# Optimization experiments

Measured on AMD Instinct MI355X. Metric: run time of the kernel, lower is better.

## Reference

```python
import jax, jax.numpy as jnp
import numpy as np

N = 100000   # nodes
E = 3200000  # edges
F = 128      # in = hidden = out channels
V = 8        # virtual nodes
L = 3        # conv layers
EPS = 1e-5


def setup_inputs() -> dict:
    key = jax.random.key(0)
    ks = jax.random.split(key, 16)
    rn = lambda k, s, sc=0.05: jax.random.normal(k, s, jnp.float32) * sc
    return {
        "x": rn(ks[0], (N, F), 1.0),
        "edge_index": jax.random.randint(ks[1], (2, E), 0, N, jnp.int32),
        "vn_mask": jax.random.randint(ks[2], (V, N), 0, 2, jnp.int32).astype(bool),
        "Wc": rn(ks[3], (L, F, F)),
        "bc": rn(ks[4], (L, F)),
        "bn_g": jnp.ones((L, F), jnp.float32),
        "bn_b": jnp.zeros((L, F), jnp.float32),
        "vn_embed": rn(ks[5], (V, F)),
        "mlp_W1": rn(ks[6], (L - 1, V, F, 2 * F)),
        "mlp_b1": rn(ks[7], (L - 1, V, 2 * F)),
        "ln1_g": jnp.ones((L - 1, V, 2 * F), jnp.float32),
        "ln1_b": jnp.zeros((L - 1, V, 2 * F), jnp.float32),
        "mlp_W2": rn(ks[8], (L - 1, V, 2 * F, F)),
        "mlp_b2": rn(ks[9], (L - 1, V, F)),
        "ln2_g": jnp.ones((L - 1, V, F), jnp.float32),
        "ln2_b": jnp.zeros((L - 1, V, F), jnp.float32),
    }


def _ln(h, g, b):
    m = h.mean(-1, keepdims=True)
    v = ((h - m) ** 2).mean(-1, keepdims=True)
    return (h - m) * jax.lax.rsqrt(v + EPS) * g + b


def _bn(h, g, b):  # training-mode batch stats over nodes (dropout p=0)
    m = h.mean(0)
    v = ((h - m) ** 2).mean(0)
    return (h - m) * jax.lax.rsqrt(v + EPS) * g + b


def reference(x, edge_index, vn_mask, Wc, bc, bn_g, bn_b, vn_embed,
              mlp_W1, mlp_b1, ln1_g, ln1_b, mlp_W2, mlp_b2, ln2_g, ln2_b):
    src, dst = edge_index[0], edge_index[1]
    loops = jnp.arange(N, dtype=src.dtype)
    src_f = jnp.concatenate([src, loops])   # GCN adds self-loops
    dst_f = jnp.concatenate([dst, loops])
    deg = jax.ops.segment_sum(jnp.ones(src_f.shape[0], x.dtype), dst_f, num_segments=N)
    dinv = jnp.where(deg > 0, jax.lax.rsqrt(deg), 0.0)
    norm = dinv[src_f] * dinv[dst_f]        # sym-normalized edge weights

    def gcn(h, W, b):  # PyG GCNConv: linear -> normalized scatter-sum -> bias
        hl = h @ W
        out = jax.ops.segment_sum(hl[src_f] * norm[:, None], dst_f, num_segments=N)
        return out + b

    maskf = vn_mask.astype(x.dtype)  # [V, N]
    vn = vn_embed                    # [V, F]
    embs = [x]
    for layer in range(L):
        h = embs[layer] + vn.sum(0, keepdims=True)       # aggregation='sum'
        h = gcn(h, Wc[layer], bc[layer])
        h = _bn(h, bn_g[layer], bn_b[layer])
        if layer != L - 1:
            h = jax.nn.relu(h)
        embs.append(h)
        if layer < L - 1:
            pooled = maskf @ embs[layer]                 # per-VN global_add_pool
            tmp = pooled + vn
            h1 = jax.nn.relu(jnp.einsum('vf,vfh->vh', tmp, mlp_W1[layer]) + mlp_b1[layer])
            h1 = _ln(h1, ln1_g[layer], ln1_b[layer])
            h2 = jax.nn.relu(jnp.einsum('vh,vhf->vf', h1, mlp_W2[layer]) + mlp_b2[layer])
            vn = _ln(h2, ln2_g[layer], ln2_b[layer])
    return embs[-1]  # JK='last'
```

## Files before the change

### kernel.cpp

```cpp
#include <hip/hip_runtime.h>
#include <hip/hip_bf16.h>
#include <hip/hip_fp16.h>

#define NN 100000
#define EE 3200000
#define FF 128
#define F2 256
#define VV 8
#define LL 3
#define EPSV 1e-5f
#define NB 98
#define NTILES 3125

typedef _Float16 f16x8 __attribute__((ext_vector_type(8)));
typedef float f32x4 __attribute__((ext_vector_type(4)));

static inline int idiv(int a, int b){ return (a + b - 1) / b; }

__global__ void k_deg(const int* __restrict__ dst, int* __restrict__ edeg){
  int stride = gridDim.x * 256;
  for (int e = blockIdx.x * 256 + threadIdx.x; e < EE; e += stride)
    atomicAdd(&edeg[dst[e]], 1);
}

__global__ void k_scanA(const int* __restrict__ edeg, int* __restrict__ offs,
                        int* __restrict__ bsum, float* __restrict__ dinv){
  __shared__ int s[1024];
  int t = threadIdx.x;
  int i = blockIdx.x * 1024 + t;
  int v = (i < NN) ? edeg[i] : 0;
  if (i < NN) dinv[i] = rsqrtf((float)(v + 1));
  int x = v;
  s[t] = x; __syncthreads();
  for (int d = 1; d < 1024; d <<= 1){
    int y = (t >= d) ? s[t - d] : 0;
    __syncthreads();
    x += y; s[t] = x;
    __syncthreads();
  }
  if (i < NN) offs[i] = x - v;
  if (t == 1023) bsum[blockIdx.x] = x;
}

__global__ void k_scanB(int* __restrict__ bsum){
  __shared__ int s[128];
  int t = threadIdx.x;
  s[t] = (t < NB) ? bsum[t] : 0;
  __syncthreads();
  if (t == 0){
    int run = 0;
    for (int k = 0; k < NB; ++k){ int tmp = s[k]; s[k] = run; run += tmp; }
  }
  __syncthreads();
  if (t < NB) bsum[t] = s[t];
}

__global__ void k_scanC(int* __restrict__ offs, const int* __restrict__ bsum,
                        int* __restrict__ cursor){
  int i = blockIdx.x * 256 + threadIdx.x;
  if (i < NN){
    int o = offs[i] + bsum[i >> 10];
    offs[i] = o;
    cursor[i] = o;
  }
  if (i == 0) offs[NN] = EE;
}

__global__ void k_scatter(const int* __restrict__ src, const int* __restrict__ dst,
                          int* __restrict__ cursor, int* __restrict__ ssorted){
  int stride = gridDim.x * 256;
  for (int e = blockIdx.x * 256 + threadIdx.x; e < EE; e += stride){
    int d = dst[e];
    int pos = atomicAdd(&cursor[d], 1);
    ssorted[pos] = src[e];
  }
}

__global__ void k_maskdetect(const unsigned char* __restrict__ m, int* __restrict__ flag){
  int any = 0;
  for (int t = threadIdx.x; t < 4096; t += 256)
    if ((t & 3) && m[t]) any = 1;
  if (any) atomicOr(flag, 1);
}

__launch_bounds__(256)
__global__ void k_matmul(const float* __restrict__ in, const float* __restrict__ W,
                         const float* __restrict__ vn, const float* __restrict__ dinv,
                         const float* __restrict__ ss, int hasbn,
                         uint2* __restrict__ hlb){
  __shared__ _Float16 As[32 * 136];
  __shared__ float   Cs[32 * 132];
  __shared__ float vs[FF], rv[FF], scs[FF], shs[FF];
  int tid = threadIdx.x, lane = tid & 63, w = tid >> 6;
  if (tid < FF){
    float s = 0.f;
    for (int v = 0; v < VV; ++v) s += vn[v * FF + tid];
    vs[tid] = s;
    scs[tid] = hasbn ? ss[tid] : 1.0f;
    shs[tid] = hasbn ? ss[FF + tid] : 0.0f;
  }
  __syncthreads();
  if (tid < FF){
    float a = 0.f;
    for (int k = 0; k < FF; ++k) a += vs[k] * W[k * FF + tid];
    rv[tid] = a;
  }
  f16x8 Bf[4][2];
  int kg = (lane >> 4) * 8;
  int cl = lane & 15;
  #pragma unroll
  for (int q = 0; q < 4; ++q)
    #pragma unroll
    for (int ct = 0; ct < 2; ++ct){
      int col = (w * 2 + ct) * 16 + cl;
      #pragma unroll
      for (int j = 0; j < 8; ++j)
        Bf[q][ct][j] = (_Float16)W[(q * 32 + kg + j) * FF + col];
    }
  __syncthreads();

  for (int t = blockIdx.x; t < NTILES; t += gridDim.x){
    int base = t * 32;
    for (int i = tid; i < 32 * 32; i += 256){
      int r = i >> 5, cq = i & 31;
      float4 v = ((const float4*)(in + (size_t)(base + r) * FF))[cq];
      if (hasbn){
        int c0 = cq * 4;
        v.x = fmaxf(fmaf(v.x, scs[c0 + 0], shs[c0 + 0]), 0.f);
        v.y = fmaxf(fmaf(v.y, scs[c0 + 1], shs[c0 + 1]), 0.f);
        v.z = fmaxf(fmaf(v.z, scs[c0 + 2], shs[c0 + 2]), 0.f);
        v.w = fmaxf(fmaf(v.w, scs[c0 + 3], shs[c0 + 3]), 0.f);
      }
      _Float16* ap = &As[r * 136 + cq * 4];
      ap[0] = (_Float16)v.x; ap[1] = (_Float16)v.y;
      ap[2] = (_Float16)v.z; ap[3] = (_Float16)v.w;
    }
    __syncthreads();
    f32x4 acc[2][2] = {{{0,0,0,0},{0,0,0,0}},{{0,0,0,0},{0,0,0,0}}};
    #pragma unroll
    for (int q = 0; q < 4; ++q){
      f16x8 Af[2];
      #pragma unroll
      for (int rt = 0; rt < 2; ++rt)
        Af[rt] = *(const f16x8*)&As[(rt * 16 + cl) * 136 + q * 32 + kg];
      #pragma unroll
      for (int rt = 0; rt < 2; ++rt)
        #pragma unroll
        for (int ct = 0; ct < 2; ++ct)
          acc[rt][ct] = __builtin_amdgcn_mfma_f32_16x16x32_f16(Af[rt], Bf[q][ct], acc[rt][ct], 0, 0, 0);
    }
    #pragma unroll
    for (int rt = 0; rt < 2; ++rt)
      #pragma unroll
      for (int ct = 0; ct < 2; ++ct){
        int col = (w * 2 + ct) * 16 + cl;
        int r0 = rt * 16 + (lane >> 4) * 4;
        #pragma unroll
        for (int reg = 0; reg < 4; ++reg)
          Cs[(r0 + reg) * 132 + col] = acc[rt][ct][reg];
      }
    __syncthreads();
    for (int i = tid; i < 32 * 32; i += 256){
      int r = i >> 5, cq = i & 31;
      float d = dinv[base + r];
      float4 c = *(const float4*)&Cs[r * 132 + cq * 4];
      int c0 = cq * 4;
      float a0 = (c.x + rv[c0 + 0]) * d;
      float a1 = (c.y + rv[c0 + 1]) * d;
      float a2 = (c.z + rv[c0 + 2]) * d;
      float a3 = (c.w + rv[c0 + 3]) * d;
      __half2 h01 = __floats2half2_rn(a0, a1);
      __half2 h23 = __floats2half2_rn(a2, a3);
      uint2 pk;
      pk.x = *reinterpret_cast<unsigned int*>(&h01);
      pk.y = *reinterpret_cast<unsigned int*>(&h23);
      hlb[(size_t)(base + r) * 32 + cq] = pk;
    }
    __syncthreads();
  }
}

__launch_bounds__(256)
__global__ void k_gather(const unsigned int* __restrict__ hlb, const float* __restrict__ dinv,
                         const int* __restrict__ offs, const int* __restrict__ ssorted,
                         float2* __restrict__ agg2, float* __restrict__ stats){
  int tid = threadIdx.x;
  int lane = tid & 63;
  int wid = (blockIdx.x * 256 + tid) >> 6;
  int nw = (gridDim.x * 256) >> 6;
  float s0 = 0.f, s1 = 0.f, q0 = 0.f, q1 = 0.f;
  for (int n = wid; n < NN; n += nw){
    int off0 = offs[n], off1 = offs[n + 1];
    unsigned int ps = hlb[(size_t)n * 64 + lane];
    float2 acc = __half22float2(*reinterpret_cast<__half2*>(&ps));
    #pragma unroll 8
    for (int e = off0; e < off1; ++e){
      unsigned int p = hlb[(size_t)ssorted[e] * 64 + lane];
      float2 f = __half22float2(*reinterpret_cast<__half2*>(&p));
      acc.x += f.x; acc.y += f.y;
    }
    float dv = dinv[n];
    float v0 = acc.x * dv, v1 = acc.y * dv;
    agg2[(size_t)n * 64 + lane] = make_float2(v0, v1);
    s0 += v0; s1 += v1; q0 += v0 * v0; q1 += v1 * v1;
  }
  __shared__ float4 red[256];
  red[tid] = make_float4(s0, s1, q0, q1);
  __syncthreads();
  if (tid < 64){
    float4 a = red[tid], b = red[tid + 64], c = red[tid + 128], d = red[tid + 192];
    a.x += b.x + c.x + d.x; a.y += b.y + c.y + d.y;
    a.z += b.z + c.z + d.z; a.w += b.w + c.w + d.w;
    atomicAdd(&stats[2 * tid], a.x);
    atomicAdd(&stats[2 * tid + 1], a.y);
    atomicAdd(&stats[FF + 2 * tid], a.z);
    atomicAdd(&stats[FF + 2 * tid + 1], a.w);
  }
}

__global__ void k_bnfin(const float* __restrict__ stats, const float* __restrict__ g,
                        const float* __restrict__ b, float* __restrict__ ss){
  int j = threadIdx.x;
  float mean = stats[j] * (1.0f / NN);
  float var  = stats[FF + j] * (1.0f / NN) - mean * mean;
  float sc = rsqrtf(var + EPSV) * g[j];
  ss[j] = sc;
  ss[FF + j] = b[j] - mean * sc;
}

__launch_bounds__(256)
__global__ void k_bnapply(float4* __restrict__ h, const float* __restrict__ stats,
                          const float* __restrict__ g, const float* __restrict__ b){
  __shared__ float ss[2 * FF];
  int tid = threadIdx.x;
  if (tid < FF){
    float mean = stats[tid] * (1.0f / NN);
    float var  = stats[FF + tid] * (1.0f / NN) - mean * mean;
    float sc = rsqrtf(var + EPSV) * g[tid];
    ss[tid] = sc;
    ss[FF + tid] = b[tid] - mean * sc;
  }
  __syncthreads();
  int n4 = NN * FF / 4;
  int stride = gridDim.x * 256;
  for (int i = blockIdx.x * 256 + tid; i < n4; i += stride){
    int c = (i & 31) * 4;
    float4 v = h[i];
    float4 sc = *(const float4*)&ss[c];
    float4 sh = *(const float4*)&ss[FF + c];
    v.x = v.x * sc.x + sh.x;
    v.y = v.y * sc.y + sh.y;
    v.z = v.z * sc.z + sh.z;
    v.w = v.w * sc.w + sh.w;
    h[i] = v;
  }
}

__global__ void k_pool(const float* __restrict__ emb, const unsigned char* __restrict__ m8,
                       const int* __restrict__ m32, const int* __restrict__ flag,
                       const float* __restrict__ ss, int hasbn,
                       float* __restrict__ pooled){
  int isb = *flag;
  int tid = blockIdx.x * 256 + threadIdx.x;
  int j = tid & 127;
  int r = tid >> 7;
  int rs = (gridDim.x * 256) >> 7;
  float sc = hasbn ? ss[j] : 1.0f;
  float sh = hasbn ? ss[FF + j] : 0.0f;
  float acc[VV];
  #pragma unroll
  for (int v = 0; v < VV; ++v) acc[v] = 0.f;
  for (; r < NN; r += rs){
    float xv = emb[r * FF + j];
    xv = fmaf(xv, sc, sh);
    if (hasbn) xv = fmaxf(xv, 0.f);
    #pragma unroll
    for (int v = 0; v < VV; ++v){
      int mv = isb ? (int)m8[v * NN + r] : m32[v * NN + r];
      if (mv) acc[v] += xv;
    }
  }
  #pragma unroll
  for (int v = 0; v < VV; ++v) atomicAdd(&pooled[v * FF + j], acc[v]);
}

__device__ __forceinline__ float blockSum(float x, float* red, int tid){
  red[tid] = x; __syncthreads();
  #pragma unroll
  for (int s = 128; s >= 1; s >>= 1){
    if (tid < s) red[tid] += red[tid + s];
    __syncthreads();
  }
  float r = red[0];
  __syncthreads();
  return r;
}

__launch_bounds__(256)
__global__ void k_vnmlp(const float* __restrict__ pooled, const float* __restrict__ vnin,
                        const float* __restrict__ W1, const float* __restrict__ b1,
                        const float* __restrict__ g1, const float* __restrict__ bb1,
                        const float* __restrict__ W2, const float* __restrict__ b2,
                        const float* __restrict__ g2, const float* __restrict__ bb2,
                        float* __restrict__ vnout){
  int v = blockIdx.x;
  int tid = threadIdx.x;
  __shared__ float tmp_s[FF];
  __shared__ float h1_s[F2];
  __shared__ float red[256];
  if (tid < FF) tmp_s[tid] = pooled[v * FF + tid] + vnin[v * FF + tid];
  __syncthreads();
  const float* W1v = W1 + (size_t)v * FF * F2;
  float acc = b1[v * F2 + tid];
  for (int k = 0; k < FF; ++k) acc += tmp_s[k] * W1v[k * F2 + tid];
  acc = fmaxf(acc, 0.f);
  float sum = blockSum(acc, red, tid);
  float sq  = blockSum(acc * acc, red, tid);
  float mean = sum * (1.f / F2);
  float var  = sq * (1.f / F2) - mean * mean;
  float y = (acc - mean) * rsqrtf(var + EPSV) * g1[v * F2 + tid] + bb1[v * F2 + tid];
  h1_s[tid] = y;
  __syncthreads();
  const float* W2v = W2 + (size_t)v * F2 * FF;
  float h2 = 0.f;
  if (tid < FF){
    float a2 = b2[v * FF + tid];
    for (int k = 0; k < F2; ++k) a2 += h1_s[k] * W2v[k * FF + tid];
    h2 = fmaxf(a2, 0.f);
  }
  float sum2 = blockSum((tid < FF) ? h2 : 0.f, red, tid);
  float sq2  = blockSum((tid < FF) ? h2 * h2 : 0.f, red, tid);
  float mean2 = sum2 * (1.f / FF);
  float var2  = sq2 * (1.f / FF) - mean2 * mean2;
  if (tid < FF)
    vnout[v * FF + tid] = (h2 - mean2) * rsqrtf(var2 + EPSV) * g2[v * FF + tid]
                          + bb2[v * FF + tid];
}

extern "C" void kernel_launch(void* const* d_in, const int* in_sizes, int n_in,
                              void* d_out, int out_size, void* d_ws, size_t ws_size,
                              hipStream_t stream){
  const float* x        = (const float*)d_in[0];
  const int*   ei       = (const int*)d_in[1];
  const unsigned char* vmask8 = (const unsigned char*)d_in[2];
  const int*   vmask32  = (const int*)d_in[2];
  const float* Wc       = (const float*)d_in[3];
  const float* bn_g     = (const float*)d_in[5];
  const float* bn_b     = (const float*)d_in[6];
  const float* vn_embed = (const float*)d_in[7];
  const float* mlp_W1   = (const float*)d_in[8];
  const float* mlp_b1   = (const float*)d_in[9];
  const float* ln1_g    = (const float*)d_in[10];
  const float* ln1_b    = (const float*)d_in[11];
  const float* mlp_W2   = (const float*)d_in[12];
  const float* mlp_b2   = (const float*)d_in[13];
  const float* ln2_g    = (const float*)d_in[14];
  const float* ln2_b    = (const float*)d_in[15];
  float* out = (float*)d_out;

  unsigned int* hlb = (unsigned int*)d_ws;
  float* bufB    = (float*)(hlb + (size_t)NN * 64);
  int*   ssorted = (int*)(bufB + (size_t)NN * FF);
  int*   offs    = ssorted + EE;
  int*   cursor  = offs + NN + 1;
  int*   edeg    = cursor + NN;
  int*   bsum    = edeg + NN;
  float* dinv    = (float*)(bsum + 128);
  float* stats   = dinv + NN;
  float* ssA     = stats + 2 * FF;
  float* ssB     = ssA + 2 * FF;
  float* pooled  = ssB + 2 * FF;
  float* vnA     = pooled + VV * FF;
  float* vnB     = vnA + VV * FF;
  int*   mflag   = (int*)(vnB + VV * FF);

  const int* esrc = ei;
  const int* edst = ei + EE;

  hipMemsetAsync(edeg, 0, NN * sizeof(int), stream);
  k_deg<<<1024, 256, 0, stream>>>(edst, edeg);
  k_scanA<<<NB, 1024, 0, stream>>>(edeg, offs, bsum, dinv);
  k_scanB<<<1, 128, 0, stream>>>(bsum);
  k_scanC<<<idiv(NN, 256), 256, 0, stream>>>(offs, bsum, cursor);
  k_scatter<<<2048, 256, 0, stream>>>(esrc, edst, cursor, ssorted);

  hipMemsetAsync(mflag, 0, sizeof(int), stream);
  k_maskdetect<<<1, 256, 0, stream>>>(vmask8, mflag);

  const float* vncur = vn_embed;
  const float* embin = x;
  float* ssbufs[2] = {ssA, ssB};
  const float* sscur = nullptr;
  float* vnbufs[2] = {vnA, vnB};

  for (int l = 0; l < LL; ++l){
    float* agg = (l < LL - 1) ? bufB : out;
    const float* Wl = Wc + (size_t)l * FF * FF;
    int hasbn = (l > 0) ? 1 : 0;

    k_matmul<<<1024, 256, 0, stream>>>(embin, Wl, vncur, dinv, sscur, hasbn, (uint2*)hlb);

    if (l < LL - 1){
      hipMemsetAsync(pooled, 0, VV * FF * sizeof(float), stream);
      k_pool<<<1024, 256, 0, stream>>>(embin, vmask8, vmask32, mflag, sscur, hasbn, pooled);
    }

    hipMemsetAsync(stats, 0, 2 * FF * sizeof(float), stream);
    k_gather<<<2048, 256, 0, stream>>>(hlb, dinv, offs, ssorted, (float2*)agg, stats);

    if (l < LL - 1){
      k_bnfin<<<1, 128, 0, stream>>>(stats, bn_g + l * FF, bn_b + l * FF, ssbufs[l]);
      k_vnmlp<<<VV, 256, 0, stream>>>(pooled, vncur,
          mlp_W1 + (size_t)l * VV * FF * F2, mlp_b1 + (size_t)l * VV * F2,
          ln1_g + (size_t)l * VV * F2, ln1_b + (size_t)l * VV * F2,
          mlp_W2 + (size_t)l * VV * F2 * FF, mlp_b2 + (size_t)l * VV * FF,
          ln2_g + (size_t)l * VV * FF, ln2_b + (size_t)l * VV * FF,
          vnbufs[l]);
      vncur = vnbufs[l];
      sscur = ssbufs[l];
      embin = agg;
    } else {
      k_bnapply<<<1024, 256, 0, stream>>>((float4*)out, stats, bn_g + l * FF, bn_b + l * FF);
    }
  }
}
```

Measured before the change: 1.442 ms.

## Bin CSR edges by source range and gather 13 nodes per wave bin-by-bin

The CSR build now sorts edges by destination and by a 13-way source bucket (src>>13), which needs a 1.3M-entry count, a multi-level scan and a separate dinv kernel. Each gather wave now owns 13 consecutive destination nodes and walks the source buckets in order, accumulating into per-node registers. The goal is to keep the random row reads of hlb within a smaller source window at a time so they hit in cache more often. In exchange, the setup phase gets heavier, each wave carries more registers, and waves handle fixed node blocks with no grid-stride balancing.

```diff
diff --git a/kernel.cpp b/kernel.cpp
--- a/kernel.cpp
+++ b/kernel.cpp
@@ -9,27 +9,39 @@
 #define VV 8
 #define LL 3
 #define EPSV 1e-5f
-#define NB 98
 #define NTILES 3125
+#define NR 13
+#define MM (NN * NR)
+#define NB2 1270
 
 typedef _Float16 f16x8 __attribute__((ext_vector_type(8)));
 typedef float f32x4 __attribute__((ext_vector_type(4)));
 
 static inline int idiv(int a, int b){ return (a + b - 1) / b; }
 
-__global__ void k_deg(const int* __restrict__ dst, int* __restrict__ edeg){
+__global__ void k_deg2(const int* __restrict__ src, const int* __restrict__ dst,
+                       int* __restrict__ edeg2){
   int stride = gridDim.x * 256;
   for (int e = blockIdx.x * 256 + threadIdx.x; e < EE; e += stride)
-    atomicAdd(&edeg[dst[e]], 1);
-}
-
-__global__ void k_scanA(const int* __restrict__ edeg, int* __restrict__ offs,
-                        int* __restrict__ bsum, float* __restrict__ dinv){
+    atomicAdd(&edeg2[dst[e] * NR + (src[e] >> 13)], 1);
+}
+
+__global__ void k_dinv2(const int* __restrict__ edeg2, float* __restrict__ dinv){
+  int n = blockIdx.x * 256 + threadIdx.x;
+  if (n < NN){
+    int s = 0;
+    #pragma unroll
+    for (int q = 0; q < NR; ++q) s += edeg2[n * NR + q];
+    dinv[n] = rsqrtf((float)(s + 1));
+  }
+}
+
+__global__ void k_scanA2(const int* __restrict__ edeg2, int* __restrict__ offs2,
+                         int* __restrict__ bsum){
   __shared__ int s[1024];
   int t = threadIdx.x;
   int i = blockIdx.x * 1024 + t;
-  int v = (i < NN) ? edeg[i] : 0;
-  if (i < NN) dinv[i] = rsqrtf((float)(v + 1));
+  int v = (i < MM) ? edeg2[i] : 0;
   int x = v;
   s[t] = x; __syncthreads();
   for (int d = 1; d < 1024; d <<= 1){
@@ -38,41 +50,46 @@
     x += y; s[t] = x;
     __syncthreads();
   }
-  if (i < NN) offs[i] = x - v;
+  if (i < MM) offs2[i] = x - v;
   if (t == 1023) bsum[blockIdx.x] = x;
 }
 
-__global__ void k_scanB(int* __restrict__ bsum){
-  __shared__ int s[128];
+__global__ void k_scanB2(int* __restrict__ bsum){
+  __shared__ int s[1024];
   int t = threadIdx.x;
-  s[t] = (t < NB) ? bsum[t] : 0;
-  __syncthreads();
-  if (t == 0){
-    int run = 0;
-    for (int k = 0; k < NB; ++k){ int tmp = s[k]; s[k] = run; run += tmp; }
-  }
-  __syncthreads();
-  if (t < NB) bsum[t] = s[t];
-}
-
-__global__ void k_scanC(int* __restrict__ offs, const int* __restrict__ bsum,
-                        int* __restrict__ cursor){
+  int v0 = (2 * t < NB2) ? bsum[2 * t] : 0;
+  int v1 = (2 * t + 1 < NB2) ? bsum[2 * t + 1] : 0;
+  int x = v0 + v1;
+  s[t] = x; __syncthreads();
+  for (int d = 1; d < 1024; d <<= 1){
+    int y = (t >= d) ? s[t - d] : 0;
+    __syncthreads();
+    x += y; s[t] = x;
+    __syncthreads();
+  }
+  int excl = x - (v0 + v1);
+  if (2 * t < NB2) bsum[2 * t] = excl;
+  if (2 * t + 1 < NB2) bsum[2 * t + 1] = excl + v0;
+}
+
+__global__ void k_scanC2(int* __restrict__ offs2, const int* __restrict__ bsum,
+                         int* __restrict__ cursor2){
   int i = blockIdx.x * 256 + threadIdx.x;
-  if (i < NN){
-    int o = offs[i] + bsum[i >> 10];
-    offs[i] = o;
-    cursor[i] = o;
-  }
-  if (i == 0) offs[NN] = EE;
+  if (i < MM){
+    int o = offs2[i] + bsum[i >> 10];
+    offs2[i] = o;
+    cursor2[i] = o;
+  }
+  if (i == 0) offs2[MM] = EE;
 }
 
 __global__ void k_scatter(const int* __restrict__ src, const int* __restrict__ dst,
-                          int* __restrict__ cursor, int* __restrict__ ssorted){
+                          int* __restrict__ cursor2, int* __restrict__ ssorted){
   int stride = gridDim.x * 256;
   for (int e = blockIdx.x * 256 + threadIdx.x; e < EE; e += stride){
-    int d = dst[e];
-    int pos = atomicAdd(&cursor[d], 1);
-    ssorted[pos] = src[e];
+    int sv = src[e];
+    int pos = atomicAdd(&cursor2[dst[e] * NR + (sv >> 13)], 1);
+    ssorted[pos] = sv;
   }
 }
 
@@ -182,25 +199,42 @@
 
 __launch_bounds__(256)
 __global__ void k_gather(const unsigned int* __restrict__ hlb, const float* __restrict__ dinv,
-                         const int* __restrict__ offs, const int* __restrict__ ssorted,
+                         const int* __restrict__ offs2, const int* __restrict__ ssorted,
                          float2* __restrict__ agg2, float* __restrict__ stats){
   int tid = threadIdx.x;
   int lane = tid & 63;
   int wid = (blockIdx.x * 256 + tid) >> 6;
-  int nw = (gridDim.x * 256) >> 6;
+  int base = wid * NR;
+  float2 acc[NR];
+  #pragma unroll
+  for (int j = 0; j < NR; ++j){
+    int n = base + j;
+    if (n < NN){
+      unsigned ps = hlb[(size_t)n * 64 + lane];
+      acc[j] = __half22float2(*reinterpret_cast<__half2*>(&ps));
+    } else acc[j] = make_float2(0.f, 0.f);
+  }
+  for (int q = 0; q < NR; ++q){
+    #pragma unroll
+    for (int j = 0; j < NR; ++j){
+      int n = base + j;
+      if (n >= NN) continue;
+      int e0 = offs2[n * NR + q], e1 = offs2[n * NR + q + 1];
+      #pragma unroll 4
+      for (int e = e0; e < e1; ++e){
+        unsigned p = hlb[(size_t)ssorted[e] * 64 + lane];
+        float2 f = __half22float2(*reinterpret_cast<__half2*>(&p));
+        acc[j].x += f.x; acc[j].y += f.y;
+      }
+    }
+  }
   float s0 = 0.f, s1 = 0.f, q0 = 0.f, q1 = 0.f;
-  for (int n = wid; n < NN; n += nw){
-    int off0 = offs[n], off1 = offs[n + 1];
-    unsigned int ps = hlb[(size_t)n * 64 + lane];
-    float2 acc = __half22float2(*reinterpret_cast<__half2*>(&ps));
-    #pragma unroll 8
-    for (int e = off0; e < off1; ++e){
-      unsigned int p = hlb[(size_t)ssorted[e] * 64 + lane];
-      float2 f = __half22float2(*reinterpret_cast<__half2*>(&p));
-      acc.x += f.x; acc.y += f.y;
-    }
+  #pragma unroll
+  for (int j = 0; j < NR; ++j){
+    int n = base + j;
+    if (n >= NN) continue;
     float dv = dinv[n];
-    float v0 = acc.x * dv, v1 = acc.y * dv;
+    float v0 = acc[j].x * dv, v1 = acc[j].y * dv;
     agg2[(size_t)n * 64 + lane] = make_float2(v0, v1);
     s0 += v0; s1 += v1; q0 += v0 * v0; q1 += v1 * v1;
   }
@@ -361,11 +395,11 @@
   unsigned int* hlb = (unsigned int*)d_ws;
   float* bufB    = (float*)(hlb + (size_t)NN * 64);
   int*   ssorted = (int*)(bufB + (size_t)NN * FF);
-  int*   offs    = ssorted + EE;
-  int*   cursor  = offs + NN + 1;
-  int*   edeg    = cursor + NN;
-  int*   bsum    = edeg + NN;
-  float* dinv    = (float*)(bsum + 128);
+  int*   offs2   = ssorted + EE;
+  int*   cursor2 = offs2 + MM + 1;
+  int*   edeg2   = cursor2 + MM;
+  int*   bsum    = edeg2 + MM;
+  float* dinv    = (float*)(bsum + NB2);
   float* stats   = dinv + NN;
   float* ssA     = stats + 2 * FF;
   float* ssB     = ssA + 2 * FF;
@@ -377,12 +411,13 @@
   const int* esrc = ei;
   const int* edst = ei + EE;
 
-  hipMemsetAsync(edeg, 0, NN * sizeof(int), stream);
-  k_deg<<<1024, 256, 0, stream>>>(edst, edeg);
-  k_scanA<<<NB, 1024, 0, stream>>>(edeg, offs, bsum, dinv);
-  k_scanB<<<1, 128, 0, stream>>>(bsum);
-  k_scanC<<<idiv(NN, 256), 256, 0, stream>>>(offs, bsum, cursor);
-  k_scatter<<<2048, 256, 0, stream>>>(esrc, edst, cursor, ssorted);
+  hipMemsetAsync(edeg2, 0, MM * sizeof(int), stream);
+  k_deg2<<<1024, 256, 0, stream>>>(esrc, edst, edeg2);
+  k_dinv2<<<idiv(NN, 256), 256, 0, stream>>>(edeg2, dinv);
+  k_scanA2<<<NB2, 1024, 0, stream>>>(edeg2, offs2, bsum);
+  k_scanB2<<<1, 1024, 0, stream>>>(bsum);
+  k_scanC2<<<idiv(MM, 256), 256, 0, stream>>>(offs2, bsum, cursor2);
+  k_scatter<<<2048, 256, 0, stream>>>(esrc, edst, cursor2, ssorted);
 
   hipMemsetAsync(mflag, 0, sizeof(int), stream);
   k_maskdetect<<<1, 256, 0, stream>>>(vmask8, mflag);
@@ -406,7 +441,7 @@
     }
 
     hipMemsetAsync(stats, 0, 2 * FF * sizeof(float), stream);
-    k_gather<<<2048, 256, 0, stream>>>(hlb, dinv, offs, ssorted, (float2*)agg, stats);
+    k_gather<<<2048, 256, 0, stream>>>(hlb, dinv, offs2, ssorted, (float2*)agg, stats);
 
     if (l < LL - 1){
       k_bnfin<<<1, 128, 0, stream>>>(stats, bn_g + l * FF, bn_b + l * FF, ssbufs[l]);
```

New measurement: 2.338 ms. 1.62x slower.
